# Kernel tuning notes

Hardware: AMD Instinct MI355X
Metric: run time of the kernel (lower is better)

The kernel has to match this reference:

```python
import jax, jax.numpy as jnp
import numpy as np
import math

B, S, D, H = 4, 2048, 1024, 16
DK = D // H
DFF = 1024  # FeedForward default d_ff=1024 (DecoderLayer passes only d_model)
EPS = 1e-6
SQRT_2_OVER_PI = math.sqrt(2.0 / math.pi)


def setup_inputs() -> dict:
    key = jax.random.key(0)
    ks = jax.random.split(key, 12)
    sc = 0.02
    x = jax.random.normal(ks[0], (B, S, D), dtype=jnp.float32)
    # causal look-ahead mask: 1 where attendable, 0 where masked
    mask = jnp.broadcast_to(jnp.tril(jnp.ones((S, S), dtype=jnp.int32)), (B, S, S))
    inp = {
        'x': x,
        'mask': mask,
        'Wq': jax.random.normal(ks[1], (D, D), jnp.float32) * sc,
        'bq': jnp.zeros((D,), jnp.float32),
        'Wk': jax.random.normal(ks[2], (D, D), jnp.float32) * sc,
        'bk': jnp.zeros((D,), jnp.float32),
        'Wv': jax.random.normal(ks[3], (D, D), jnp.float32) * sc,
        'bv': jnp.zeros((D,), jnp.float32),
        'Wo': jax.random.normal(ks[4], (D, D), jnp.float32) * sc,
        'bo': jnp.zeros((D,), jnp.float32),
        'W1': jax.random.normal(ks[5], (D, DFF), jnp.float32) * sc,
        'b1': jnp.zeros((DFF,), jnp.float32),
        'W2': jax.random.normal(ks[6], (DFF, D), jnp.float32) * sc,
        'b2': jnp.zeros((D,), jnp.float32),
        'alpha1': jnp.ones((D,), jnp.float32),
        'bias1': jnp.zeros((D,), jnp.float32),
        'alpha2': jnp.ones((D,), jnp.float32),
        'bias2': jnp.zeros((D,), jnp.float32),
    }
    return inp


def _norm(x, alpha, bias):
    # torch: (x - mean) / (x.std(unbiased=True) + eps) * alpha + bias
    mean = jnp.mean(x, axis=-1, keepdims=True)
    var = jnp.sum((x - mean) ** 2, axis=-1, keepdims=True) / (x.shape[-1] - 1)
    std = jnp.sqrt(var)
    return alpha * (x - mean) / (std + EPS) + bias


def _gelu(x):
    return 0.5 * x * (1.0 + jnp.tanh(SQRT_2_OVER_PI * (x + 0.044715 * x ** 3)))


def reference(x, mask, Wq, bq, Wk, bk, Wv, bv, Wo, bo, W1, b1, W2, b2,
              alpha1, bias1, alpha2, bias2):
    b, s, d = x.shape
    x2 = _norm(x, alpha1, bias1)
    q = (x2 @ Wq + bq).reshape(b, s, H, DK).transpose(0, 2, 1, 3)  # bhsd
    k = (x2 @ Wk + bk).reshape(b, s, H, DK).transpose(0, 2, 1, 3)
    v = (x2 @ Wv + bv).reshape(b, s, H, DK).transpose(0, 2, 1, 3)
    scores = jnp.einsum('bhqd,bhkd->bhqk', q, k) / jnp.sqrt(jnp.float32(DK))
    scores = jnp.where(mask[:, None, :, :] == 0, jnp.float32(-1e9), scores)
    probs = jax.nn.softmax(scores, axis=-1)
    attn = jnp.einsum('bhqk,bhkd->bhqd', probs, v)
    concat = attn.transpose(0, 2, 1, 3).reshape(b, s, d)
    x = x + (concat @ Wo + bo)
    x2 = _norm(x, alpha2, bias2)
    ff = _gelu(x2 @ W1 + b1) @ W2 + b2
    return x + ff
```

## Files before the change

### kernel.cpp

```cpp
#include <hip/hip_runtime.h>
#include <hip/hip_bf16.h>
#include <math.h>


#define B_ 4
#define S_ 2048
#define D_ 1024
#define H_ 16
#define DFF_ 1024
#define BUFS 24576

typedef __attribute__((ext_vector_type(8))) short short8;
typedef __attribute__((ext_vector_type(8))) unsigned short ushort8;
typedef __attribute__((ext_vector_type(4))) float f32x4;

__device__ __forceinline__ unsigned short f2bf(float f) {
  __hip_bfloat16 h = __float2bfloat16(f);
  return *reinterpret_cast<unsigned short*>(&h);
}

__device__ __forceinline__ void gload16(const void* g, void* l) {
  __builtin_amdgcn_global_load_lds(
      (const __attribute__((address_space(1))) void*)g,
      (__attribute__((address_space(3))) void*)l, 16, 0, 0);
}

__global__ __launch_bounds__(256) void prep_k(
    const float* s0, const float* s1, const float* s2, const float* s3,
    const float* s4, const float* s5, unsigned short* d0, unsigned short* d1,
    unsigned short* d2, unsigned short* d3, unsigned short* d4,
    unsigned short* d5, const float* __restrict__ x,
    const float* __restrict__ alpha, const float* __restrict__ bias,
    unsigned short* __restrict__ xout) {
  __shared__ float tile[64][65];
  const int bid = blockIdx.x;
  const int t = threadIdx.x;
  if (bid < 1536) {
    const int z = bid >> 8, rem = bid & 255;
    const int k0 = (rem >> 4) * 64, n0 = (rem & 15) * 64;
    const float* src;
    unsigned short* dst;
    switch (z) {
      case 0: src = s0; dst = d0; break;
      case 1: src = s1; dst = d1; break;
      case 2: src = s2; dst = d2; break;
      case 3: src = s3; dst = d3; break;
      case 4: src = s4; dst = d4; break;
      default: src = s5; dst = d5; break;
    }
    const int r = t >> 2, c0 = (t & 3) * 16;
    const float4* sp = reinterpret_cast<const float4*>(
        src + (size_t)(k0 + r) * 1024 + n0 + c0);
#pragma unroll
    for (int j = 0; j < 4; ++j) {
      float4 v = sp[j];
      tile[r][c0 + 4 * j] = v.x;
      tile[r][c0 + 4 * j + 1] = v.y;
      tile[r][c0 + 4 * j + 2] = v.z;
      tile[r][c0 + 4 * j + 3] = v.w;
    }
    __syncthreads();
    ushort8 o0, o1;
#pragma unroll
    for (int j = 0; j < 8; ++j) o0[j] = f2bf(tile[c0 + j][r]);
#pragma unroll
    for (int j = 0; j < 8; ++j) o1[j] = f2bf(tile[c0 + 8 + j][r]);
    unsigned short* dp = dst + (size_t)(n0 + r) * 1024 + k0 + c0;
    *reinterpret_cast<ushort8*>(dp) = o0;
    *reinterpret_cast<ushort8*>(dp + 8) = o1;
  } else {
    const int w = t >> 6, lane = t & 63;
    const int row = (bid - 1536) * 4 + w;
    const float4* xp = reinterpret_cast<const float4*>(x + (size_t)row * D_);
    const float4* ap = reinterpret_cast<const float4*>(alpha);
    const float4* bp = reinterpret_cast<const float4*>(bias);
    float4 v[4];
    float s = 0.0f, q = 0.0f;
#pragma unroll
    for (int j = 0; j < 4; ++j) {
      v[j] = xp[lane + 64 * j];
      s += v[j].x + v[j].y + v[j].z + v[j].w;
      q += v[j].x * v[j].x + v[j].y * v[j].y + v[j].z * v[j].z +
           v[j].w * v[j].w;
    }
#pragma unroll
    for (int off = 1; off < 64; off <<= 1) {
      s += __shfl_xor(s, off);
      q += __shfl_xor(q, off);
    }
    const float mean = s * (1.0f / D_);
    const float var = fmaxf((q - D_ * mean * mean) * (1.0f / (D_ - 1)), 0.0f);
    const float inv = 1.0f / (sqrtf(var) + 1e-6f);
    ushort4* op = reinterpret_cast<ushort4*>(xout + (size_t)row * D_);
#pragma unroll
    for (int j = 0; j < 4; ++j) {
      float4 a = ap[lane + 64 * j];
      float4 b = bp[lane + 64 * j];
      ushort4 o;
      o.x = f2bf((v[j].x - mean) * inv * a.x + b.x);
      o.y = f2bf((v[j].y - mean) * inv * a.y + b.y);
      o.z = f2bf((v[j].z - mean) * inv * a.z + b.z);
      o.w = f2bf((v[j].w - mean) * inv * a.w + b.w);
      op[lane + 64 * j] = o;
    }
  }
}

__global__ __launch_bounds__(256) void ln_k(const float* __restrict__ x,
                                            const float* __restrict__ alpha,
                                            const float* __restrict__ bias,
                                            unsigned short* __restrict__ out) {
  const int w = threadIdx.x >> 6, lane = threadIdx.x & 63;
  const int row = blockIdx.x * 4 + w;
  const float4* xp = reinterpret_cast<const float4*>(x + (size_t)row * D_);
  const float4* ap = reinterpret_cast<const float4*>(alpha);
  const float4* bp = reinterpret_cast<const float4*>(bias);
  float4 v[4];
  float s = 0.0f, q = 0.0f;
#pragma unroll
  for (int j = 0; j < 4; ++j) {
    v[j] = xp[lane + 64 * j];
    s += v[j].x + v[j].y + v[j].z + v[j].w;
    q += v[j].x * v[j].x + v[j].y * v[j].y + v[j].z * v[j].z + v[j].w * v[j].w;
  }
#pragma unroll
  for (int off = 1; off < 64; off <<= 1) {
    s += __shfl_xor(s, off);
    q += __shfl_xor(q, off);
  }
  const float mean = s * (1.0f / D_);
  const float var = fmaxf((q - D_ * mean * mean) * (1.0f / (D_ - 1)), 0.0f);
  const float inv = 1.0f / (sqrtf(var) + 1e-6f);
  ushort4* op = reinterpret_cast<ushort4*>(out + (size_t)row * D_);
#pragma unroll
  for (int j = 0; j < 4; ++j) {
    float4 a = ap[lane + 64 * j];
    float4 b = bp[lane + 64 * j];
    ushort4 o;
    o.x = f2bf((v[j].x - mean) * inv * a.x + b.x);
    o.y = f2bf((v[j].y - mean) * inv * a.y + b.y);
    o.z = f2bf((v[j].z - mean) * inv * a.z + b.z);
    o.w = f2bf((v[j].w - mean) * inv * a.w + b.w);
    op[lane + 64 * j] = o;
  }
}

__device__ __forceinline__ void gemm_core8p(
    const unsigned short* __restrict__ A, const unsigned short* __restrict__ Wt,
    int m0, int n0, int K, unsigned short* lds, f32x4 (&acc)[4][4]) {
  const int t = threadIdx.x;
  const int wv = t >> 6, lane = t & 63, quad = lane >> 4, l16 = lane & 15;
  const int wm = wv >> 1, wn = wv & 1;
  const int NT = K >> 6;

  const unsigned short* Ag[4];
  int Ao[4];
  const unsigned short* Bg[2];
  int Bo[2];
#pragma unroll
  for (int g = 0; g < 4; ++g) {
    int u = g * 512 + t, row = u >> 3, ps = u & 7;
    Ag[g] = A + (size_t)(m0 + row) * K + ((ps ^ (row & 7)) << 3);
    Ao[g] = u * 8;
  }
#pragma unroll
  for (int g = 0; g < 2; ++g) {
    int u = g * 512 + t, row = u >> 3, ps = u & 7;
    Bg[g] = Wt + (size_t)(n0 + row) * K + ((ps ^ (row & 7)) << 3);
    Bo[g] = 16384 + u * 8;
  }

#pragma unroll
  for (int tt = 0; tt < 2; ++tt) {
    unsigned short* lb = lds + tt * BUFS;
    const int kk = tt * 64;
    gload16(Ag[0] + kk, lb + Ao[0]);
    gload16(Ag[1] + kk, lb + Ao[1]);
    gload16(Bg[0] + kk, lb + Bo[0]);
    gload16(Ag[2] + kk, lb + Ao[2]);
    gload16(Ag[3] + kk, lb + Ao[3]);
    gload16(Bg[1] + kk, lb + Bo[1]);
  }

  int cb = 0;
  for (int kt = 0; kt < NT; ++kt) {
    if (kt + 1 < NT)
      asm volatile("s_waitcnt vmcnt(6)" ::: "memory");
    else
      asm volatile("s_waitcnt vmcnt(0)" ::: "memory");
    asm volatile("s_barrier" ::: "memory");

    const unsigned short* Ab = lds + cb * BUFS;
    const unsigned short* Bb = Ab + 16384;
    int sbf = cb + 2;
    if (sbf >= 3) sbf -= 3;
    unsigned short* sb = lds + sbf * BUFS;
    const int kk2 = (kt + 2) << 6;
    const bool st = (kt + 2 < NT);

    {
      short8 af[4], bf[4];
#pragma unroll
      for (int mt = 0; mt < 4; ++mt) {
        int r = wm * 64 + mt * 16 + l16;
        af[mt] = *reinterpret_cast<const short8*>(
            &Ab[r * 64 + ((quad ^ (r & 7)) << 3)]);
      }
#pragma unroll
      for (int nt = 0; nt < 4; ++nt) {
        int r = wn * 64 + nt * 16 + l16;
        bf[nt] = *reinterpret_cast<const short8*>(
            &Bb[r * 64 + ((quad ^ (r & 7)) << 3)]);
      }
      if (st) {
        gload16(Ag[0] + kk2, sb + Ao[0]);
        gload16(Ag[1] + kk2, sb + Ao[1]);
        gload16(Bg[0] + kk2, sb + Bo[0]);
      }
      __builtin_amdgcn_sched_barrier(0);
      __builtin_amdgcn_s_setprio(1);
#pragma unroll
      for (int mt = 0; mt < 4; ++mt)
#pragma unroll
        for (int nt = 0; nt < 4; ++nt)
          acc[mt][nt] = __builtin_amdgcn_mfma_f32_16x16x32_bf16(
              af[mt], bf[nt], acc[mt][nt], 0, 0, 0);
      __builtin_amdgcn_s_setprio(0);
      __builtin_amdgcn_sched_barrier(0);
    }
    {
      short8 af[4], bf[4];
#pragma unroll
      for (int mt = 0; mt < 4; ++mt) {
        int r = wm * 64 + mt * 16 + l16;
        af[mt] = *reinterpret_cast<const short8*>(
            &Ab[r * 64 + (((4 + quad) ^ (r & 7)) << 3)]);
      }
#pragma unroll
      for (int nt = 0; nt < 4; ++nt) {
        int r = wn * 64 + nt * 16 + l16;
        bf[nt] = *reinterpret_cast<const short8*>(
            &Bb[r * 64 + (((4 + quad) ^ (r & 7)) << 3)]);
      }
      if (st) {
        gload16(Ag[2] + kk2, sb + Ao[2]);
        gload16(Ag[3] + kk2, sb + Ao[3]);
        gload16(Bg[1] + kk2, sb + Bo[1]);
      }
      __builtin_amdgcn_sched_barrier(0);
      __builtin_amdgcn_s_setprio(1);
#pragma unroll
      for (int mt = 0; mt < 4; ++mt)
#pragma unroll
        for (int nt = 0; nt < 4; ++nt)
          acc[mt][nt] = __builtin_amdgcn_mfma_f32_16x16x32_bf16(
              af[mt], bf[nt], acc[mt][nt], 0, 0, 0);
      __builtin_amdgcn_s_setprio(0);
      __builtin_amdgcn_sched_barrier(0);
    }
    asm volatile("s_barrier" ::: "memory");
    cb = (cb + 1 == 3) ? 0 : cb + 1;
  }
}

__global__ __launch_bounds__(512, 2) void gemm_k(
    const unsigned short* __restrict__ A, const unsigned short* __restrict__ Wt,
    const float* __restrict__ bias, const float* __restrict__ res,
    void* __restrict__ outp, int M, int N, int K, int flags) {
  extern __shared__ unsigned short lds[];
  const int t = threadIdx.x;
  const int bid = blockIdx.x;
  const int xcd = bid & 7, loc = bid >> 3;
  const int n_blk = loc >> 2;
  const int m_blk = xcd * 4 + (loc & 3);
  const int m0 = m_blk * 256, n0 = n_blk * 128;
  const int wv = t >> 6, lane = t & 63, quad = lane >> 4, l16 = lane & 15;
  const int wm = wv >> 1, wn = wv & 1;
  f32x4 acc[4][4] = {};
  gemm_core8p(A, Wt, m0, n0, K, lds, acc);

  const bool obf = flags & 1, dog = flags & 2;
#pragma unroll
  for (int nt = 0; nt < 4; ++nt) {
    int col = n0 + wn * 64 + nt * 16 + l16;
    float bv = bias[col];
#pragma unroll
    for (int mt = 0; mt < 4; ++mt) {
#pragma unroll
      for (int r = 0; r < 4; ++r) {
        int row = m0 + wm * 64 + mt * 16 + quad * 4 + r;
        float v = acc[mt][nt][r] + bv;
        if (res) v += res[(size_t)row * N + col];
        if (dog) {
          float e = __expf(1.5957691216057308f * (v + 0.044715f * v * v * v));
          float th = 1.0f - 2.0f / (1.0f + e);
          v = 0.5f * v * (1.0f + th);
        }
        if (obf)
          ((unsigned short*)outp)[(size_t)row * N + col] = f2bf(v);
        else
          ((float*)outp)[(size_t)row * N + col] = v;
      }
    }
  }
}

__global__ __launch_bounds__(512, 2) void gemmqkv_k(
    const unsigned short* __restrict__ A, const unsigned short* __restrict__ Wt,
    const float* __restrict__ bq, const float* __restrict__ bk,
    const float* __restrict__ bv, unsigned short* __restrict__ outq,
    unsigned short* __restrict__ outk, unsigned short* __restrict__ outvt,
    int M, int K) {
  extern __shared__ unsigned short lds[];
  const int t = threadIdx.x;
  const int bid = blockIdx.x;
  const int xcd = bid & 7, loc = bid >> 3;
  const int n_blk = loc >> 2;
  const int m_blk = xcd * 4 + (loc & 3);
  const int m0 = m_blk * 256, n0 = n_blk * 128;
  const int wv = t >> 6, lane = t & 63, quad = lane >> 4, l16 = lane & 15;
  const int wm = wv >> 1, wn = wv & 1;
  f32x4 acc[4][4] = {};
  gemm_core8p(A, Wt, m0, n0, K, lds, acc);

  const int seg = n0 >> 10;
  const int nb = n0 & 1023;
  const float* bias = (seg == 0) ? bq : (seg == 1) ? bk : bv;
  if (seg < 2) {
    unsigned short* o = (seg == 0) ? outq : outk;
#pragma unroll
    for (int nt = 0; nt < 4; ++nt) {
      int col = nb + wn * 64 + nt * 16 + l16;
      float bvv = bias[col];
#pragma unroll
      for (int mt = 0; mt < 4; ++mt)
#pragma unroll
        for (int r = 0; r < 4; ++r) {
          int row = m0 + wm * 64 + mt * 16 + quad * 4 + r;
          o[(size_t)row * D_ + col] = f2bf(acc[mt][nt][r] + bvv);
        }
    }
  } else {
#pragma unroll
    for (int nt = 0; nt < 4; ++nt) {
      int col = nb + wn * 64 + nt * 16 + l16;
      float bvv = bias[col];
      int h = col >> 6, dk = col & 63;
#pragma unroll
      for (int mt = 0; mt < 4; ++mt) {
        int m = m0 + wm * 64 + mt * 16 + quad * 4;
        int b = m >> 11, sidx = m & 2047;
        ushort4 o;
        o.x = f2bf(acc[mt][nt][0] + bvv);
        o.y = f2bf(acc[mt][nt][1] + bvv);
        o.z = f2bf(acc[mt][nt][2] + bvv);
        o.w = f2bf(acc[mt][nt][3] + bvv);
        *reinterpret_cast<ushort4*>(
            &outvt[(((size_t)(b * 16 + h) * 64 + dk) * 2048 + sidx)]) = o;
      }
    }
  }
}

__global__ __launch_bounds__(256, 3) void attn_k(
    const unsigned short* __restrict__ Q, const unsigned short* __restrict__ Kg,
    const unsigned short* __restrict__ VT, unsigned short* __restrict__ Og) {
  __shared__ unsigned short Ks[2][64 * 64];
  __shared__ unsigned short Vs[2][64 * 64];
  __shared__ unsigned short Ps[4 * 16 * 72];
  const int t = threadIdx.x;
  const int qt = 31 - (blockIdx.x >> 6);
  const int bh = blockIdx.x & 63;
  const int b = bh >> 4, h = bh & 15;
  const int w = t >> 6, lane = t & 63, quad = lane >> 4, l16 = lane & 15;
  const int q0 = qt * 64 + w * 16;
  unsigned short* PsW = &Ps[w * 16 * 72];

  short8 qf[2];
#pragma unroll
  for (int kc = 0; kc < 2; ++kc)
    qf[kc] = *reinterpret_cast<const short8*>(
        Q + (size_t)(b * S_ + q0 + l16) * D_ + h * 64 + kc * 32 + quad * 8);
  asm volatile("" ::"v"(qf[0]), "v"(qf[1]) : "memory");

  f32x4 Oh[4] = {};
  f32x4 sums = {};
  short8 onev;
#pragma unroll
  for (int j = 0; j < 8; ++j) onev[j] = (short)0x3F80;

  const int srA = w * 8 + (lane >> 3);
  const int ssA = ((lane & 7) ^ (srA & 7)) * 8;
  const int srB = srA + 32;
  const int ssB = ((lane & 7) ^ (srB & 7)) * 8;
  const unsigned short* KgA = Kg + (size_t)(b * S_ + srA) * D_ + h * 64 + ssA;
  const unsigned short* KgB = Kg + (size_t)(b * S_ + srB) * D_ + h * 64 + ssB;
  const unsigned short* VgA = VT + ((size_t)bh * 64 + srA) * 2048 + ssA;
  const unsigned short* VgB = VT + ((size_t)bh * 64 + srB) * 2048 + ssB;
  unsigned short* KlA = &Ks[0][(w * 8) * 64];
  unsigned short* KlB = &Ks[0][(32 + w * 8) * 64];
  unsigned short* VlA = &Vs[0][(w * 8) * 64];
  unsigned short* VlB = &Vs[0][(32 + w * 8) * 64];

  const float C0 = 0.18033688011f;
  const float C1 = -23.08312065f;

  gload16(KgA, KlA);
  gload16(KgB, KlB);
  gload16(VgA, VlA);
  gload16(VgB, VlB);
  KgA += (size_t)64 * D_;
  KgB += (size_t)64 * D_;
  VgA += 64;
  VgB += 64;

  for (int kt = 0; kt <= qt; ++kt) {
    const bool diag = (kt == qt);
    const int coff = (kt & 1) << 12;
    const int noff = ((kt & 1) ^ 1) << 12;

    if (kt < qt) {
      gload16(KgA, KlA + noff);
      gload16(KgB, KlB + noff);
      gload16(VgA, VlA + noff);
      gload16(VgB, VlB + noff);
      KgA += (size_t)64 * D_;
      KgB += (size_t)64 * D_;
      VgA += 64;
      VgB += 64;
      asm volatile("s_waitcnt vmcnt(4)" ::: "memory");
    } else {
      asm volatile("s_waitcnt vmcnt(0)" ::: "memory");
    }
    asm volatile("s_barrier" ::: "memory");

    const unsigned short* Ksc = &Ks[0][coff];
    const unsigned short* Vsc = &Vs[0][coff];

    f32x4 sch[4] = {};
    __builtin_amdgcn_s_setprio(1);
#pragma unroll
    for (int mt = 0; mt < 4; ++mt) {
      int r = mt * 16 + l16;
      short8 kf0 = *reinterpret_cast<const short8*>(
          &Ksc[r * 64 + ((quad ^ (r & 7)) << 3)]);
      short8 kf1 = *reinterpret_cast<const short8*>(
          &Ksc[r * 64 + (((4 + quad) ^ (r & 7)) << 3)]);
      sch[mt] = __builtin_amdgcn_mfma_f32_16x16x32_bf16(kf0, qf[0], sch[mt],
                                                        0, 0, 0);
      sch[mt] = __builtin_amdgcn_mfma_f32_16x16x32_bf16(kf1, qf[1], sch[mt],
                                                        0, 0, 0);
    }
    __builtin_amdgcn_s_setprio(0);

    {
      const int kb0 = kt * 64;
      const int q = q0 + l16;
#pragma unroll
      for (int mt = 0; mt < 4; ++mt) {
        float pv[4];
#pragma unroll
        for (int r = 0; r < 4; ++r) {
          int key = kb0 + mt * 16 + quad * 4 + r;
          float p = __builtin_amdgcn_exp2f(fmaf(sch[mt][r], C0, C1));
          if (diag && key > q) p = 0.0f;
          pv[r] = p;
        }
        ushort4 pk = {f2bf(pv[0]), f2bf(pv[1]), f2bf(pv[2]), f2bf(pv[3])};
        *reinterpret_cast<ushort4*>(&PsW[l16 * 72 + mt * 16 + quad * 4]) = pk;
      }
    }
    __builtin_amdgcn_sched_barrier(0);

    short8 pf[2];
#pragma unroll
    for (int kc = 0; kc < 2; ++kc)
      pf[kc] = *reinterpret_cast<const short8*>(
          &PsW[l16 * 72 + kc * 32 + quad * 8]);

    __builtin_amdgcn_s_setprio(1);
#pragma unroll
    for (int kc = 0; kc < 2; ++kc) {
      sums = __builtin_amdgcn_mfma_f32_16x16x32_bf16(pf[kc], onev, sums,
                                                     0, 0, 0);
#pragma unroll
      for (int nd = 0; nd < 4; ++nd) {
        int r = nd * 16 + l16;
        short8 vf = *reinterpret_cast<const short8*>(
            &Vsc[r * 64 + (((kc * 4 + quad) ^ (r & 7)) << 3)]);
        Oh[nd] = __builtin_amdgcn_mfma_f32_16x16x32_bf16(pf[kc], vf, Oh[nd],
                                                         0, 0, 0);
      }
    }
    __builtin_amdgcn_s_setprio(0);
    asm volatile("s_barrier" ::: "memory");
  }

#pragma unroll
  for (int r = 0; r < 4; ++r) {
    float rl = 1.0f / sums[r];
#pragma unroll
    for (int nd = 0; nd < 4; ++nd)
      Og[(size_t)(b * S_ + q0 + quad * 4 + r) * D_ + h * 64 + nd * 16 + l16] =
          f2bf(Oh[nd][r] * rl);
  }
}

extern "C" void kernel_launch(void* const* d_in, const int* in_sizes, int n_in,
                              void* d_out, int out_size, void* d_ws,
                              size_t ws_size, hipStream_t stream) {
  const float* x = (const float*)d_in[0];
  const float* Wq = (const float*)d_in[2];
  const float* bq = (const float*)d_in[3];
  const float* Wk = (const float*)d_in[4];
  const float* bk = (const float*)d_in[5];
  const float* Wv = (const float*)d_in[6];
  const float* bv = (const float*)d_in[7];
  const float* Wo = (const float*)d_in[8];
  const float* bo = (const float*)d_in[9];
  const float* W1 = (const float*)d_in[10];
  const float* b1 = (const float*)d_in[11];
  const float* W2 = (const float*)d_in[12];
  const float* b2 = (const float*)d_in[13];
  const float* alpha1 = (const float*)d_in[14];
  const float* bias1 = (const float*)d_in[15];
  const float* alpha2 = (const float*)d_in[16];
  const float* bias2 = (const float*)d_in[17];
  float* out = (float*)d_out;

  char* ws = (char*)d_ws;
  const size_t MB = 1024 * 1024;
  unsigned short* wqT = (unsigned short*)(ws + 0 * MB);
  unsigned short* wkT = (unsigned short*)(ws + 2 * MB);
  unsigned short* wvT = (unsigned short*)(ws + 4 * MB);
  unsigned short* woT = (unsigned short*)(ws + 6 * MB);
  unsigned short* w1T = (unsigned short*)(ws + 8 * MB);
  unsigned short* w2T = (unsigned short*)(ws + 10 * MB);
  unsigned short* x2a = (unsigned short*)(ws + 12 * MB);
  unsigned short* qb = (unsigned short*)(ws + 28 * MB);
  unsigned short* kb = (unsigned short*)(ws + 44 * MB);
  unsigned short* vtb = (unsigned short*)(ws + 60 * MB);

  static bool attr_set = false;
  if (!attr_set) {
    attr_set = true;
    (void)hipFuncSetAttribute((const void*)gemm_k,
                              hipFuncAttributeMaxDynamicSharedMemorySize,
                              147456);
    (void)hipFuncSetAttribute((const void*)gemmqkv_k,
                              hipFuncAttributeMaxDynamicSharedMemorySize,
                              147456);
  }

  const int M = B_ * S_;

  prep_k<<<dim3(1536 + M / 4), dim3(256), 0, stream>>>(
      Wq, Wk, Wv, Wo, W1, W2, wqT, wkT, wvT, woT, w1T, w2T, x, alpha1, bias1,
      x2a);

  gemmqkv_k<<<dim3(768), dim3(512), 147456, stream>>>(x2a, wqT, bq, bk, bv,
                                                      qb, kb, vtb, M, D_);

  attn_k<<<dim3(2048), dim3(256), 0, stream>>>(qb, kb, vtb, x2a);

  gemm_k<<<dim3(256), dim3(512), 147456, stream>>>(x2a, woT, bo, x, out, M,
                                                   D_, D_, 0);

  ln_k<<<dim3(M / 4), dim3(256), 0, stream>>>(out, alpha2, bias2, qb);

  gemm_k<<<dim3(256), dim3(512), 147456, stream>>>(qb, w1T, b1, nullptr, kb,
                                                   M, DFF_, D_, 3);

  gemm_k<<<dim3(256), dim3(512), 147456, stream>>>(kb, w2T, b2, out, out, M,
                                                   D_, DFF_, 0);
}
```

Measured before the change: 392.2 us.

## Widen attention blocks to 128 queries and specialize GEMM kernels per use

The attention kernel now uses 8 waves covering 128 query rows per block instead of 4 waves over 64. Each K/V tile is loaded into LDS once and reused by twice as many query rows, and each thread issues half the global-to-LDS loads. Waves whose query rows lie entirely before the current key tile skip compute but still join the barriers, which adds some idle time on the last tile. The generic GEMM kernel is also split into three specialized kernels with compile-time epilogue flags, removing runtime branching on the GELU and bf16-output options.

```diff
diff --git a/kernel.cpp b/kernel.cpp
--- a/kernel.cpp
+++ b/kernel.cpp
@@ -263,11 +263,11 @@
   }
 }
 
-__global__ __launch_bounds__(512, 2) void gemm_k(
+__device__ __forceinline__ void gemm_body(
     const unsigned short* __restrict__ A, const unsigned short* __restrict__ Wt,
     const float* __restrict__ bias, const float* __restrict__ res,
-    void* __restrict__ outp, int M, int N, int K, int flags) {
-  extern __shared__ unsigned short lds[];
+    void* __restrict__ outp, int M, int N, int K, bool obf, bool dog,
+    unsigned short* lds) {
   const int t = threadIdx.x;
   const int bid = blockIdx.x;
   const int xcd = bid & 7, loc = bid >> 3;
@@ -279,7 +279,6 @@
   f32x4 acc[4][4] = {};
   gemm_core8p(A, Wt, m0, n0, K, lds, acc);
 
-  const bool obf = flags & 1, dog = flags & 2;
 #pragma unroll
   for (int nt = 0; nt < 4; ++nt) {
     int col = n0 + wn * 64 + nt * 16 + l16;
@@ -303,6 +302,28 @@
       }
     }
   }
+}
+
+__global__ __launch_bounds__(512, 2) void gemm_wo_k(
+    const unsigned short* __restrict__ A, const unsigned short* __restrict__ Wt,
+    const float* __restrict__ bias, const float* __restrict__ res,
+    void* __restrict__ outp, int M, int N, int K) {
+  extern __shared__ unsigned short lds[];
+  gemm_body(A, Wt, bias, res, outp, M, N, K, false, false, lds);
+}
+__global__ __launch_bounds__(512, 2) void gemm_w1_k(
+    const unsigned short* __restrict__ A, const unsigned short* __restrict__ Wt,
+    const float* __restrict__ bias, const float* __restrict__ res,
+    void* __restrict__ outp, int M, int N, int K) {
+  extern __shared__ unsigned short lds[];
+  gemm_body(A, Wt, bias, res, outp, M, N, K, true, true, lds);
+}
+__global__ __launch_bounds__(512, 2) void gemm_w2_k(
+    const unsigned short* __restrict__ A, const unsigned short* __restrict__ Wt,
+    const float* __restrict__ bias, const float* __restrict__ res,
+    void* __restrict__ outp, int M, int N, int K) {
+  extern __shared__ unsigned short lds[];
+  gemm_body(A, Wt, bias, res, outp, M, N, K, false, false, lds);
 }
 
 __global__ __launch_bounds__(512, 2) void gemmqkv_k(
@@ -362,18 +383,19 @@
   }
 }
 
-__global__ __launch_bounds__(256, 3) void attn_k(
+__global__ __launch_bounds__(512, 6) void attn_k(
     const unsigned short* __restrict__ Q, const unsigned short* __restrict__ Kg,
     const unsigned short* __restrict__ VT, unsigned short* __restrict__ Og) {
   __shared__ unsigned short Ks[2][64 * 64];
   __shared__ unsigned short Vs[2][64 * 64];
-  __shared__ unsigned short Ps[4 * 16 * 72];
+  __shared__ unsigned short Ps[8 * 16 * 72];
   const int t = threadIdx.x;
-  const int qt = 31 - (blockIdx.x >> 6);
+  const int pb = 15 - (blockIdx.x >> 6);
   const int bh = blockIdx.x & 63;
   const int b = bh >> 4, h = bh & 15;
   const int w = t >> 6, lane = t & 63, quad = lane >> 4, l16 = lane & 15;
-  const int q0 = qt * 64 + w * 16;
+  const int q0 = pb * 128 + w * 16;
+  const int qw = q0 >> 6;
   unsigned short* PsW = &Ps[w * 16 * 72];
 
   short8 qf[2];
@@ -391,44 +413,31 @@
 
   const int srA = w * 8 + (lane >> 3);
   const int ssA = ((lane & 7) ^ (srA & 7)) * 8;
-  const int srB = srA + 32;
-  const int ssB = ((lane & 7) ^ (srB & 7)) * 8;
   const unsigned short* KgA = Kg + (size_t)(b * S_ + srA) * D_ + h * 64 + ssA;
-  const unsigned short* KgB = Kg + (size_t)(b * S_ + srB) * D_ + h * 64 + ssB;
   const unsigned short* VgA = VT + ((size_t)bh * 64 + srA) * 2048 + ssA;
-  const unsigned short* VgB = VT + ((size_t)bh * 64 + srB) * 2048 + ssB;
   unsigned short* KlA = &Ks[0][(w * 8) * 64];
-  unsigned short* KlB = &Ks[0][(32 + w * 8) * 64];
   unsigned short* VlA = &Vs[0][(w * 8) * 64];
-  unsigned short* VlB = &Vs[0][(32 + w * 8) * 64];
 
   const float C0 = 0.18033688011f;
   const float C1 = -23.08312065f;
 
+  const int ntm1 = 2 * pb + 1;
+
   gload16(KgA, KlA);
-  gload16(KgB, KlB);
   gload16(VgA, VlA);
-  gload16(VgB, VlB);
   KgA += (size_t)64 * D_;
-  KgB += (size_t)64 * D_;
   VgA += 64;
-  VgB += 64;
-
-  for (int kt = 0; kt <= qt; ++kt) {
-    const bool diag = (kt == qt);
+
+  for (int kt = 0; kt <= ntm1; ++kt) {
     const int coff = (kt & 1) << 12;
     const int noff = ((kt & 1) ^ 1) << 12;
 
-    if (kt < qt) {
+    if (kt < ntm1) {
       gload16(KgA, KlA + noff);
-      gload16(KgB, KlB + noff);
       gload16(VgA, VlA + noff);
-      gload16(VgB, VlB + noff);
       KgA += (size_t)64 * D_;
-      KgB += (size_t)64 * D_;
       VgA += 64;
-      VgB += 64;
-      asm volatile("s_waitcnt vmcnt(4)" ::: "memory");
+      asm volatile("s_waitcnt vmcnt(2)" ::: "memory");
     } else {
       asm volatile("s_waitcnt vmcnt(0)" ::: "memory");
     }
@@ -436,63 +445,68 @@
 
     const unsigned short* Ksc = &Ks[0][coff];
     const unsigned short* Vsc = &Vs[0][coff];
-
-    f32x4 sch[4] = {};
-    __builtin_amdgcn_s_setprio(1);
-#pragma unroll
-    for (int mt = 0; mt < 4; ++mt) {
-      int r = mt * 16 + l16;
-      short8 kf0 = *reinterpret_cast<const short8*>(
-          &Ksc[r * 64 + ((quad ^ (r & 7)) << 3)]);
-      short8 kf1 = *reinterpret_cast<const short8*>(
-          &Ksc[r * 64 + (((4 + quad) ^ (r & 7)) << 3)]);
-      sch[mt] = __builtin_amdgcn_mfma_f32_16x16x32_bf16(kf0, qf[0], sch[mt],
-                                                        0, 0, 0);
-      sch[mt] = __builtin_amdgcn_mfma_f32_16x16x32_bf16(kf1, qf[1], sch[mt],
-                                                        0, 0, 0);
-    }
-    __builtin_amdgcn_s_setprio(0);
-
-    {
-      const int kb0 = kt * 64;
-      const int q = q0 + l16;
+    const bool act = (kt <= qw);
+    const bool diag = (kt == qw);
+
+    if (act) {
+      f32x4 sch[4] = {};
+      __builtin_amdgcn_s_setprio(1);
 #pragma unroll
       for (int mt = 0; mt < 4; ++mt) {
-        float pv[4];
-#pragma unroll
-        for (int r = 0; r < 4; ++r) {
-          int key = kb0 + mt * 16 + quad * 4 + r;
-          float p = __builtin_amdgcn_exp2f(fmaf(sch[mt][r], C0, C1));
-          if (diag && key > q) p = 0.0f;
-          pv[r] = p;
+        int r = mt * 16 + l16;
+        short8 kf0 = *reinterpret_cast<const short8*>(
+            &Ksc[r * 64 + ((quad ^ (r & 7)) << 3)]);
+        short8 kf1 = *reinterpret_cast<const short8*>(
+            &Ksc[r * 64 + (((4 + quad) ^ (r & 7)) << 3)]);
+        sch[mt] = __builtin_amdgcn_mfma_f32_16x16x32_bf16(kf0, qf[0], sch[mt],
+                                                          0, 0, 0);
+        sch[mt] = __builtin_amdgcn_mfma_f32_16x16x32_bf16(kf1, qf[1], sch[mt],
+                                                          0, 0, 0);
+      }
+      __builtin_amdgcn_s_setprio(0);
+
+      {
+        const int kb0 = kt * 64;
+        const int q = q0 + l16;
+#pragma unroll
+        for (int mt = 0; mt < 4; ++mt) {
+          float pv[4];
+#pragma unroll
+          for (int r = 0; r < 4; ++r) {
+            int key = kb0 + mt * 16 + quad * 4 + r;
+            float p = __builtin_amdgcn_exp2f(fmaf(sch[mt][r], C0, C1));
+            if (diag && key > q) p = 0.0f;
+            pv[r] = p;
+          }
+          ushort4 pk = {f2bf(pv[0]), f2bf(pv[1]), f2bf(pv[2]), f2bf(pv[3])};
+          *reinterpret_cast<ushort4*>(&PsW[l16 * 72 + mt * 16 + quad * 4]) =
+              pk;
         }
-        ushort4 pk = {f2bf(pv[0]), f2bf(pv[1]), f2bf(pv[2]), f2bf(pv[3])};
-        *reinterpret_cast<ushort4*>(&PsW[l16 * 72 + mt * 16 + quad * 4]) = pk;
-      }
-    }
-    __builtin_amdgcn_sched_barrier(0);
-
-    short8 pf[2];
-#pragma unroll
-    for (int kc = 0; kc < 2; ++kc)
-      pf[kc] = *reinterpret_cast<const short8*>(
-          &PsW[l16 * 72 + kc * 32 + quad * 8]);
-
-    __builtin_amdgcn_s_setprio(1);
-#pragma unroll
-    for (int kc = 0; kc < 2; ++kc) {
-      sums = __builtin_amdgcn_mfma_f32_16x16x32_bf16(pf[kc], onev, sums,
-                                                     0, 0, 0);
-#pragma unroll
-      for (int nd = 0; nd < 4; ++nd) {
-        int r = nd * 16 + l16;
-        short8 vf = *reinterpret_cast<const short8*>(
-            &Vsc[r * 64 + (((kc * 4 + quad) ^ (r & 7)) << 3)]);
-        Oh[nd] = __builtin_amdgcn_mfma_f32_16x16x32_bf16(pf[kc], vf, Oh[nd],
-                                                         0, 0, 0);
-      }
-    }
-    __builtin_amdgcn_s_setprio(0);
+      }
+      __builtin_amdgcn_sched_barrier(0);
+
+      short8 pf[2];
+#pragma unroll
+      for (int kc = 0; kc < 2; ++kc)
+        pf[kc] = *reinterpret_cast<const short8*>(
+            &PsW[l16 * 72 + kc * 32 + quad * 8]);
+
+      __builtin_amdgcn_s_setprio(1);
+#pragma unroll
+      for (int kc = 0; kc < 2; ++kc) {
+        sums = __builtin_amdgcn_mfma_f32_16x16x32_bf16(pf[kc], onev, sums,
+                                                       0, 0, 0);
+#pragma unroll
+        for (int nd = 0; nd < 4; ++nd) {
+          int r = nd * 16 + l16;
+          short8 vf = *reinterpret_cast<const short8*>(
+              &Vsc[r * 64 + (((kc * 4 + quad) ^ (r & 7)) << 3)]);
+          Oh[nd] = __builtin_amdgcn_mfma_f32_16x16x32_bf16(pf[kc], vf, Oh[nd],
+                                                           0, 0, 0);
+        }
+      }
+      __builtin_amdgcn_s_setprio(0);
+    }
     asm volatile("s_barrier" ::: "memory");
   }
 
@@ -544,7 +558,13 @@
   static bool attr_set = false;
   if (!attr_set) {
     attr_set = true;
-    (void)hipFuncSetAttribute((const void*)gemm_k,
+    (void)hipFuncSetAttribute((const void*)gemm_wo_k,
+                              hipFuncAttributeMaxDynamicSharedMemorySize,
+                              147456);
+    (void)hipFuncSetAttribute((const void*)gemm_w1_k,
+                              hipFuncAttributeMaxDynamicSharedMemorySize,
+                              147456);
+    (void)hipFuncSetAttribute((const void*)gemm_w2_k,
                               hipFuncAttributeMaxDynamicSharedMemorySize,
                               147456);
     (void)hipFuncSetAttribute((const void*)gemmqkv_k,
@@ -561,16 +581,16 @@
   gemmqkv_k<<<dim3(768), dim3(512), 147456, stream>>>(x2a, wqT, bq, bk, bv,
                                                       qb, kb, vtb, M, D_);
 
-  attn_k<<<dim3(2048), dim3(256), 0, stream>>>(qb, kb, vtb, x2a);
-
-  gemm_k<<<dim3(256), dim3(512), 147456, stream>>>(x2a, woT, bo, x, out, M,
-                                                   D_, D_, 0);
+  attn_k<<<dim3(1024), dim3(512), 0, stream>>>(qb, kb, vtb, x2a);
+
+  gemm_wo_k<<<dim3(256), dim3(512), 147456, stream>>>(x2a, woT, bo, x, out, M,
+                                                      D_, D_);
 
   ln_k<<<dim3(M / 4), dim3(256), 0, stream>>>(out, alpha2, bias2, qb);
 
-  gemm_k<<<dim3(256), dim3(512), 147456, stream>>>(qb, w1T, b1, nullptr, kb,
-                                                   M, DFF_, D_, 3);
-
-  gemm_k<<<dim3(256), dim3(512), 147456, stream>>>(kb, w2T, b2, out, out, M,
-                                                   D_, DFF_, 0);
-}
+  gemm_w1_k<<<dim3(256), dim3(512), 147456, stream>>>(qb, w1T, b1, nullptr,
+                                                      kb, M, DFF_, D_);
+
+  gemm_w2_k<<<dim3(256), dim3(512), 147456, stream>>>(kb, w2T, b2, out, out,
+                                                      M, D_, DFF_);
+}
```

After: 395.9 us. No clear change (+0.9%).
